# Kernel optimization log

Hardware: AMD Instinct MI355X
Metric: run time of the kernel (lower is better)

The kernel has to match this reference:

```python
import jax, jax.numpy as jnp
import numpy as np

B, T, D, H, L, F, V, BANDS = 16, 512, 1024, 8, 6, 4096, 30000, 16
RES = [1, 1, 2, 2, 4, 4, 8, 8]  # per-head K/V resolution schedule
HD = D // H


def setup_inputs() -> dict:
    key = jax.random.key(0)
    ks = iter(jax.random.split(key, 64))
    s = 0.02
    p = {
        "tokens": jax.random.randint(next(ks), (B, T), 0, V, dtype=jnp.int32),
        "embed": jax.random.normal(next(ks), (V, D), jnp.float32) * s,
        "pos_embed": jax.random.normal(next(ks), (T, D), jnp.float32) * s,
        "Wq": jax.random.normal(next(ks), (L, D, D), jnp.float32) * s,
        "bq": jnp.zeros((L, D), jnp.float32),
        "Wk": jax.random.normal(next(ks), (L, D, D), jnp.float32) * s,
        "bk": jnp.zeros((L, D), jnp.float32),
        "Wv": jax.random.normal(next(ks), (L, D, D), jnp.float32) * s,
        "bv": jnp.zeros((L, D), jnp.float32),
        "Wo": jax.random.normal(next(ks), (L, D, D), jnp.float32) * s,
        "bo": jnp.zeros((L, D), jnp.float32),
        "ln1_g": jnp.ones((L, D), jnp.float32),
        "ln1_b": jnp.zeros((L, D), jnp.float32),
        "ln2_g": jnp.ones((L, D), jnp.float32),
        "ln2_b": jnp.zeros((L, D), jnp.float32),
        "W1": jax.random.normal(next(ks), (L, D, F), jnp.float32) * s,
        "b1": jnp.zeros((L, F), jnp.float32),
        "W2": jax.random.normal(next(ks), (L, F, D), jnp.float32) * s,
        "b2": jnp.zeros((L, D), jnp.float32),
        "gates": jnp.ones((L, H, BANDS), jnp.float32),
        "lnf_g": jnp.ones((D,), jnp.float32),
        "lnf_b": jnp.zeros((D,), jnp.float32),
    }
    return p


def _ln(x, g, b, eps=1e-5):
    mu = jnp.mean(x, -1, keepdims=True)
    var = jnp.var(x, -1, keepdims=True)
    return (x - mu) * jax.lax.rsqrt(var + eps) * g + b


def _hfa_attention(x, Wq, bq, Wk, bk, Wv, bv, Wo, bo, gates_l):
    # x: [B,T,D]; per-head resolution schedule + spectral band gating.
    q = (x @ Wq + bq).reshape(B, T, H, HD).transpose(0, 2, 1, 3)  # [B,H,T,HD]
    k = (x @ Wk + bk).reshape(B, T, H, HD).transpose(0, 2, 1, 3)
    v = (x @ Wv + bv).reshape(B, T, H, HD).transpose(0, 2, 1, 3)
    nb = T // 2 + 1
    band_of_bin = (jnp.arange(nb) * BANDS) // nb  # map rfft bin -> spectral band
    scale = 1.0 / np.sqrt(HD)
    outs = []
    for h in range(H):
        r = RES[h]
        kh = k[:, h].reshape(B, T // r, r, HD).mean(2)  # pooled keys [B,T/r,HD]
        vh = v[:, h].reshape(B, T // r, r, HD).mean(2)
        scores = jnp.einsum("btd,bsd->bts", q[:, h], kh) * scale
        attn = jax.nn.softmax(scores, axis=-1)
        o = jnp.einsum("bts,bsd->btd", attn, vh)  # [B,T,HD]
        # spectral band gating along sequence axis
        g = gates_l[h][band_of_bin]  # [nb]
        f = jnp.fft.rfft(o, axis=1) * g[None, :, None]
        o = jnp.fft.irfft(f, n=T, axis=1)
        outs.append(o)
    out = jnp.concatenate(outs, axis=-1)  # [B,T,D]
    return out @ Wo + bo


def reference(tokens, embed, pos_embed, Wq, bq, Wk, bk, Wv, bv, Wo, bo,
              ln1_g, ln1_b, ln2_g, ln2_b, W1, b1, W2, b2, gates, lnf_g, lnf_b):
    x = embed[tokens] + pos_embed[jnp.arange(T)][None, :, :]  # [B,T,D]
    for l in range(L):
        h = _ln(x, ln1_g[l], ln1_b[l])
        x = x + _hfa_attention(h, Wq[l], bq[l], Wk[l], bk[l], Wv[l], bv[l],
                               Wo[l], bo[l], gates[l])
        h = _ln(x, ln2_g[l], ln2_b[l])
        ff = jax.nn.gelu(h @ W1[l] + b1[l], approximate=False) @ W2[l] + b2[l]
        x = x + ff
    return _ln(x, lnf_g, lnf_b)
```

## Files before the change

kernel.cpp:

```cpp
#include <hip/hip_runtime.h>
#include <hip/hip_bf16.h>
#include <math.h>

#define Bn 16
#define Tn 512
#define Dn 1024
#define Hn 8
#define Ln 6
#define Fn 4096
#define HDn 128

typedef __attribute__((ext_vector_type(8))) short short8;
typedef __attribute__((ext_vector_type(4))) float f32x4;

__device__ __forceinline__ float bf2f(unsigned short u){
  union{float f; unsigned int i;} c; c.i = ((unsigned int)u)<<16; return c.f;
}
__device__ __forceinline__ unsigned short f2bf(float f){
  union{float f; unsigned int i;} c; c.f=f;
  unsigned int r = c.i + 0x7fffu + ((c.i>>16)&1u);
  return (unsigned short)(r>>16);
}

#define GLOAD(gp, lp) __builtin_amdgcn_global_load_lds( \
    (const __attribute__((address_space(1))) void*)(const void*)(gp), \
    (__attribute__((address_space(3))) void*)(void*)(lp), 16, 0, 0)

__global__ __launch_bounds__(256) void embed_kernel(
    const int* __restrict__ tok, const float* __restrict__ emb,
    const float* __restrict__ pos, float* __restrict__ x){
  long row = blockIdx.x;
  int t = (int)(row & (Tn-1));
  int tk = tok[row];
  int d = threadIdx.x*4;
  float4 e = *(const float4*)(emb + (long)tk*Dn + d);
  float4 p = *(const float4*)(pos + (long)t*Dn + d);
  float4 r; r.x=e.x+p.x; r.y=e.y+p.y; r.z=e.z+p.z; r.w=e.w+p.w;
  *(float4*)(x + row*(long)Dn + d) = r;
}

template<int OUTBF>
__global__ __launch_bounds__(256) void ln_kernel(
    const float* __restrict__ x, const float* __restrict__ g,
    const float* __restrict__ b, void* __restrict__ outp){
  long row = blockIdx.x;
  const float* xr = x + row*(long)Dn;
  int tid = threadIdx.x;
  float4 v4 = *(const float4*)(xr + tid*4);
  float s  = v4.x+v4.y+v4.z+v4.w;
  float s2 = v4.x*v4.x + v4.y*v4.y + v4.z*v4.z + v4.w*v4.w;
  #pragma unroll
  for (int o=32;o;o>>=1){ s += __shfl_xor(s,o); s2 += __shfl_xor(s2,o); }
  __shared__ float rs[4], rs2[4];
  int w = tid>>6;
  if ((tid&63)==0){ rs[w]=s; rs2[w]=s2; }
  __syncthreads();
  s  = rs[0]+rs[1]+rs[2]+rs[3];
  s2 = rs2[0]+rs2[1]+rs2[2]+rs2[3];
  float mu  = s*(1.f/Dn);
  float var = s2*(1.f/Dn) - mu*mu;
  float rstd = rsqrtf(var + 1e-5f);
  float4 gg = *(const float4*)(g + tid*4);
  float4 bb = *(const float4*)(b + tid*4);
  float o0 = (v4.x-mu)*rstd*gg.x + bb.x;
  float o1 = (v4.y-mu)*rstd*gg.y + bb.y;
  float o2 = (v4.z-mu)*rstd*gg.z + bb.z;
  float o3 = (v4.w-mu)*rstd*gg.w + bb.w;
  if (OUTBF){
    unsigned short* o = (unsigned short*)outp + row*(long)Dn + tid*4;
    o[0]=f2bf(o0); o[1]=f2bf(o1); o[2]=f2bf(o2); o[3]=f2bf(o3);
  } else {
    float* o = (float*)outp + row*(long)Dn + tid*4;
    o[0]=o0; o[1]=o1; o[2]=o2; o[3]=o3;
  }
}

__global__ __launch_bounds__(256) void transpose_w(
    const float* __restrict__ W, unsigned short* __restrict__ WT, int Kd, int Nd){
  __shared__ float tile[32][33];
  long lofs = (long)blockIdx.z * Kd * Nd;
  int n0 = blockIdx.x*32, k0 = blockIdx.y*32;
  int tx = threadIdx.x & 31, ty = threadIdx.x >> 5;
  #pragma unroll
  for (int i=0;i<4;i++){
    int kk = k0 + ty + i*8;
    tile[ty+i*8][tx] = W[lofs + (long)kk*Nd + n0 + tx];
  }
  __syncthreads();
  #pragma unroll
  for (int i=0;i<4;i++){
    int nn = n0 + ty + i*8;
    WT[lofs + (long)nn*Kd + k0 + tx] = f2bf(tile[tx][ty+i*8]);
  }
}

__global__ __launch_bounds__(256) void pack_bias(
    const float* __restrict__ bq, const float* __restrict__ bk,
    const float* __restrict__ bv, float* __restrict__ bqkv){
  int i = blockIdx.x*256 + threadIdx.x;
  int l = i / (3*Dn); int r = i - l*3*Dn; int w = r / Dn; int d = r - w*Dn;
  const float* src = (w==0)? bq : ((w==1)? bk : bv);
  bqkv[i] = src[l*Dn + d];
}

__global__ __launch_bounds__(512) void ckern(
    const float* __restrict__ gates, float* __restrict__ cbuf){
  int lh = blockIdx.x;
  __shared__ float gb[16];
  if (threadIdx.x < 16) gb[threadIdx.x] = gates[lh*16 + threadIdx.x];
  __syncthreads();
  int m = threadIdx.x;
  float acc = gb[0];
  for (int j=1;j<256;j++){
    int band = (j*16)/257;
    int kmod = (j*m) & 511;
    acc += 2.f*gb[band]*cosf(1.2271846303085129e-2f * (float)kmod);
  }
  acc += gb[15] * ((m & 1) ? -1.f : 1.f);
  cbuf[lh*512 + m] = acc * (1.f/512.f);
}

__global__ __launch_bounds__(256) void gfill(
    const float* __restrict__ cbuf, unsigned short* __restrict__ G){
  long idx = (long)blockIdx.x*256 + threadIdx.x;
  int lh = (int)(idx >> 18);
  int rem = (int)(idx & 262143);
  int t = rem >> 9, s = rem & 511;
  G[idx] = f2bf(cbuf[lh*512 + ((t - s) & 511)]);
}

__global__ __launch_bounds__(256) void pool_kernel(
    const unsigned short* __restrict__ kin, const unsigned short* __restrict__ vin,
    unsigned short* __restrict__ kp, unsigned short* __restrict__ vTp){
  long idx = (long)blockIdx.x*256 + threadIdx.x;
  if (idx >= (long)Bn*1920*HDn) return;
  long rem = idx; int hh = 0; int S = 512;
  for (hh=0; hh<8; hh++){
    S = 512 >> (hh>>1);
    long seg = (long)Bn*S*HDn;
    if (rem < seg) break;
    rem -= seg;
  }
  int r = 512 / S;
  int d = (int)(rem % HDn);
  long t2 = rem / HDn;
  int s = (int)(t2 % S);
  int b = (int)(t2 / S);
  const unsigned short* kb = kin + ((long)(b*Tn + s*r))*Dn + hh*HDn + d;
  const unsigned short* vb = vin + ((long)(b*Tn + s*r))*Dn + hh*HDn + d;
  float ks=0.f, vs=0.f;
  for (int j=0;j<r;j++){ ks += bf2f(kb[(long)j*Dn]); vs += bf2f(vb[(long)j*Dn]); }
  float inv = 1.f/(float)r;
  int pref=0;
  for (int g2=0; g2<hh; g2++) pref += 512 >> (g2>>1);
  long segb = (long)Bn*HDn*pref;
  kp [segb + ((long)b*S + s)*HDn + d] = f2bf(ks*inv);
  vTp[segb + ((long)b*HDn + d)*S + s] = f2bf(vs*inv);
}

template<int S>
__global__ __launch_bounds__(64) void softmax_kernel(
    const float* __restrict__ sc, unsigned short* __restrict__ at){
  const int NV = S/64;
  long row = blockIdx.x;
  const float* r = sc + row*(long)S;
  int lane = threadIdx.x;
  float vals[NV];
  float mx = -1e30f;
  #pragma unroll
  for (int i=0;i<NV;i++){ vals[i] = r[lane + i*64] * 0.08838834764831845f; mx = fmaxf(mx, vals[i]); }
  #pragma unroll
  for (int o=32;o;o>>=1) mx = fmaxf(mx, __shfl_xor(mx, o));
  float sum = 0.f;
  #pragma unroll
  for (int i=0;i<NV;i++){ vals[i] = expf(vals[i]-mx); sum += vals[i]; }
  #pragma unroll
  for (int o=32;o;o>>=1) sum += __shfl_xor(sum, o);
  float inv = 1.f/sum;
  #pragma unroll
  for (int i=0;i<NV;i++) at[row*(long)S + lane + i*64] = f2bf(vals[i]*inv);
}

template<int MODE>
__global__ __launch_bounds__(256)
void gemm_kernel(const unsigned short* __restrict__ A, int lda, long sAb, long sAh,
                 const unsigned short* __restrict__ Bt, int ldb, long sBb, long sBh,
                 void* __restrict__ Cout, int ldc, long sCb, long sCh,
                 const float* __restrict__ bias, long sbias,
                 int zshift, int zmask,
                 int M, int N, int K)
{
  __shared__ unsigned short AB[2][2][128*64];
  int z = blockIdx.z;
  int zb = z & zmask, zh = z >> zshift;
  const unsigned short* Az = A + (long)zb*sAb + (long)zh*sAh;
  const unsigned short* Bz = Bt + (long)zb*sBb + (long)zh*sBh;
  const float* biasz = bias ? (bias + (long)zh*sbias) : nullptr;
  int m0 = blockIdx.y*128, n0 = blockIdx.x*128;
  int tid = threadIdx.x;
  int lane = tid & 63, wid = tid >> 6;
  int wm = wid >> 1, wn = wid & 1;
  f32x4 zero4 = {0.f,0.f,0.f,0.f};
  f32x4 acc[4][4];
  #pragma unroll
  for (int m=0;m<4;m++)
    #pragma unroll
    for (int n=0;n<4;n++)
      acc[m][n] = zero4;
  const int r16 = lane & 15, kq = lane >> 4;

  auto stage = [&](int buf, int k0){
    #pragma unroll
    for (int i=0;i<4;i++){
      int chunk = i*256 + tid;
      int row = chunk >> 3, c = chunk & 7;
      int cg = (c ^ (row & 7)) * 8;
      int gm = m0 + row; gm = gm < M ? gm : M-1;
      GLOAD(Az + (long)gm*lda + k0 + cg, AB[buf][0] + (i*256 + wid*64)*8);
    }
    #pragma unroll
    for (int i=0;i<4;i++){
      int chunk = i*256 + tid;
      int row = chunk >> 3, c = chunk & 7;
      int cg = (c ^ (row & 7)) * 8;
      int gn = n0 + row; gn = gn < N ? gn : N-1;
      GLOAD(Bz + (long)gn*ldb + k0 + cg, AB[buf][1] + (i*256 + wid*64)*8);
    }
  };

  int NT = K >> 6;
  stage(0, 0);
  for (int t = 0; t < NT; t++){
    if (t + 1 < NT){
      stage((t+1)&1, (t+1)*64);
      asm volatile("s_waitcnt vmcnt(8)" ::: "memory");
    } else {
      asm volatile("s_waitcnt vmcnt(0)" ::: "memory");
    }
    __builtin_amdgcn_s_barrier();
    const unsigned short* As = AB[t&1][0];
    const unsigned short* Bs = AB[t&1][1];
    #pragma unroll
    for (int kk=0; kk<64; kk+=32){
      short8 af[4], bfr[4];
      int kb = (kk + kq*8) * 2;
      #pragma unroll
      for (int m=0;m<4;m++){
        int row = wm*64 + m*16 + r16;
        af[m] = *(const short8*)((const char*)As + row*128 + (kb ^ ((row & 7) << 4)));
      }
      #pragma unroll
      for (int n=0;n<4;n++){
        int row = wn*64 + n*16 + r16;
        bfr[n] = *(const short8*)((const char*)Bs + row*128 + (kb ^ ((row & 7) << 4)));
      }
      #pragma unroll
      for (int m=0;m<4;m++)
        #pragma unroll
        for (int n=0;n<4;n++)
          acc[m][n] = __builtin_amdgcn_mfma_f32_16x16x32_bf16(af[m], bfr[n], acc[m][n], 0, 0, 0);
    }
    __builtin_amdgcn_s_barrier();
  }
  #pragma unroll
  for (int n=0;n<4;n++){
    int col = n0 + wn*64 + n*16 + r16;
    if (col >= N) continue;
    float bvv = 0.f;
    if (MODE != 0 && biasz != nullptr) bvv = biasz[col];
    #pragma unroll
    for (int m=0;m<4;m++){
      #pragma unroll
      for (int e=0;e<4;e++){
        int row = m0 + wm*64 + m*16 + kq*4 + e;
        if (row >= M) continue;
        float vv = acc[m][n][e] + bvv;
        long cidx = (long)zb*sCb + (long)zh*sCh + (long)row*ldc + col;
        if (MODE == 0)      ((float*)Cout)[cidx] = vv;
        else                ((unsigned short*)Cout)[cidx] = f2bf(vv);
      }
    }
  }
}

template<int MODE, int Mt, int Nt, int Kt, long SBH, long SCH, int BIASST>
__global__ __launch_bounds__(256)
void gemm_big(const unsigned short* __restrict__ A,
              const unsigned short* __restrict__ Bt,
              void* __restrict__ Cout,
              const float* __restrict__ bias)
{
  __shared__ char shraw[2][32768];
  int zh = blockIdx.z;
  const unsigned short* Bz = Bt + (long)zh*SBH;
  const float* biasz = bias + (long)zh*BIASST;
  constexpr int gx = Nt/128, gy = Mt/128, nwg = gx*gy;
  int lin  = blockIdx.y * gx + blockIdx.x;
  int nlin = (lin & 7) * (nwg >> 3) + (lin >> 3);
  int m0 = (nlin / gx) * 128, n0 = (nlin % gx) * 128;
  int tid = threadIdx.x;
  int lane = tid & 63, wid = tid >> 6;
  int wm = wid >> 1, wn = wid & 1;
  f32x4 zero4 = {0.f,0.f,0.f,0.f};
  f32x4 acc[4][4];
  #pragma unroll
  for (int m=0;m<4;m++)
    #pragma unroll
    for (int n=0;n<4;n++)
      acc[m][n] = zero4;
  const int r16 = lane & 15, kq = lane >> 4;

  const unsigned short* pA[4];
  const unsigned short* pB[4];
  #pragma unroll
  for (int i=0;i<4;i++){
    int chunk = i*256 + tid;
    int row = chunk >> 3, c = chunk & 7;
    int cg = (c ^ (row & 7)) * 8;
    pA[i] = A  + (long)(m0 + row)*Kt + cg;
    pB[i] = Bz + (long)(n0 + row)*Kt + cg;
  }
  auto stage = [&](int buf, int k0){
    unsigned short* As = (unsigned short*)shraw[buf];
    #pragma unroll
    for (int i=0;i<4;i++) GLOAD(pA[i] + k0, As + (i*256 + wid*64)*8);
    #pragma unroll
    for (int i=0;i<4;i++) GLOAD(pB[i] + k0, As + 8192 + (i*256 + wid*64)*8);
  };

  constexpr int NT = Kt/64;
  stage(0, 0);
  for (int t = 0; t < NT; t++){
    if (t + 1 < NT){
      stage((t+1)&1, (t+1)*64);
      asm volatile("s_waitcnt vmcnt(8)" ::: "memory");
    } else {
      asm volatile("s_waitcnt vmcnt(0)" ::: "memory");
    }
    __builtin_amdgcn_s_barrier();
    const unsigned short* As = (const unsigned short*)shraw[t&1];
    const unsigned short* Bs = As + 8192;
    #pragma unroll
    for (int kk=0; kk<64; kk+=32){
      short8 af[4], bfr[4];
      int kb = (kk + kq*8) * 2;
      #pragma unroll
      for (int m=0;m<4;m++){
        int row = wm*64 + m*16 + r16;
        af[m] = *(const short8*)((const char*)As + row*128 + (kb ^ ((row & 7) << 4)));
      }
      #pragma unroll
      for (int n=0;n<4;n++){
        int row = wn*64 + n*16 + r16;
        bfr[n] = *(const short8*)((const char*)Bs + row*128 + (kb ^ ((row & 7) << 4)));
      }
      #pragma unroll
      for (int m=0;m<4;m++)
        #pragma unroll
        for (int n=0;n<4;n++)
          acc[m][n] = __builtin_amdgcn_mfma_f32_16x16x32_bf16(af[m], bfr[n], acc[m][n], 0, 0, 0);
    }
    __builtin_amdgcn_s_barrier();
  }

  if (MODE == 1 || MODE == 2){
    unsigned short* shb = (unsigned short*)&shraw[0][0];
    #pragma unroll
    for (int n=0;n<4;n++){
      int col = wn*64 + n*16 + r16;
      float bvv = biasz[n0 + col];
      #pragma unroll
      for (int m=0;m<4;m++){
        #pragma unroll
        for (int e=0;e<4;e++){
          int row = wm*64 + m*16 + kq*4 + e;
          float vv = acc[m][n][e] + bvv;
          if (MODE == 2) vv = 0.5f*vv*(1.f + erff(vv*0.7071067811865475f));
          shb[row*136 + col] = f2bf(vv);
        }
      }
    }
    __syncthreads();
    #pragma unroll
    for (int i=0;i<8;i++){
      int chunk = i*256 + tid;
      int row = chunk >> 4, col = (chunk & 15)*8;
      short8 vv8 = *(const short8*)(shb + row*136 + col);
      *(short8*)((unsigned short*)Cout + (long)zh*SCH +
                 (long)(m0 + row)*Nt + n0 + col) = vv8;
    }
  } else {
    float* shf = (float*)&shraw[0][0];
    #pragma unroll
    for (int ph=0; ph<2; ph++){
      __syncthreads();
      if (wm == ph){
        #pragma unroll
        for (int n=0;n<4;n++){
          int col = wn*64 + n*16 + r16;
          float bvv = biasz[n0 + col];
          #pragma unroll
          for (int m=0;m<4;m++){
            #pragma unroll
            for (int e=0;e<4;e++){
              int rl = m*16 + kq*4 + e;
              shf[rl*136 + col] = acc[m][n][e] + bvv;
            }
          }
        }
      }
      __syncthreads();
      #pragma unroll
      for (int i=0;i<8;i++){
        int chunk = i*256 + tid;
        int row = chunk >> 5, col = (chunk & 31)*4;
        float4 vv = *(const float4*)(shf + row*136 + col);
        float* cp = (float*)Cout + (long)(m0 + ph*64 + row)*Nt + n0 + col;
        float4 o = *(const float4*)cp;
        o.x += vv.x; o.y += vv.y; o.z += vv.z; o.w += vv.w;
        *(float4*)cp = o;
      }
    }
  }
}

extern "C" void kernel_launch(void* const* d_in, const int* in_sizes, int n_in,
                              void* d_out, int out_size, void* d_ws, size_t ws_size,
                              hipStream_t stream){
  const int*   tokens = (const int*)  d_in[0];
  const float* embedp = (const float*)d_in[1];
  const float* pos    = (const float*)d_in[2];
  const float* Wq  = (const float*)d_in[3];
  const float* bq  = (const float*)d_in[4];
  const float* Wk  = (const float*)d_in[5];
  const float* bk  = (const float*)d_in[6];
  const float* Wv  = (const float*)d_in[7];
  const float* bv  = (const float*)d_in[8];
  const float* Wo  = (const float*)d_in[9];
  const float* bo  = (const float*)d_in[10];
  const float* ln1g= (const float*)d_in[11];
  const float* ln1b= (const float*)d_in[12];
  const float* ln2g= (const float*)d_in[13];
  const float* ln2b= (const float*)d_in[14];
  const float* W1  = (const float*)d_in[15];
  const float* b1  = (const float*)d_in[16];
  const float* W2  = (const float*)d_in[17];
  const float* b2  = (const float*)d_in[18];
  const float* gates=(const float*)d_in[19];
  const float* lnfg= (const float*)d_in[20];
  const float* lnfb= (const float*)d_in[21];
  float* out = (float*)d_out;

  char* base = (char*)d_ws;
  size_t off = 0;
  auto take = [&](size_t bytes)->char*{
    char* p = base + off;
    off = (off + bytes + 255) & ~(size_t)255;
    return p;
  };
  unsigned short* WqT = (unsigned short*)take((size_t)Ln*Dn*Dn*2);
  unsigned short* WkT = (unsigned short*)take((size_t)Ln*Dn*Dn*2);
  unsigned short* WvT = (unsigned short*)take((size_t)Ln*Dn*Dn*2);
  unsigned short* WoT = (unsigned short*)take((size_t)Ln*Dn*Dn*2);
  unsigned short* W1T = (unsigned short*)take((size_t)Ln*Dn*Fn*2);
  unsigned short* W2T = (unsigned short*)take((size_t)Ln*Dn*Fn*2);
  unsigned short* G   = (unsigned short*)take((size_t)Ln*Hn*Tn*Tn*2);
  float*          cbuf= (float*)take((size_t)Ln*Hn*Tn*4);
  float*          bqkv= (float*)take((size_t)Ln*3*Dn*4);
  float*          x   = (float*)take((size_t)Bn*Tn*Dn*4);
  unsigned short* hbuf= (unsigned short*)take((size_t)Bn*Tn*Dn*2);
  unsigned short* q   = (unsigned short*)take((size_t)Bn*Tn*Dn*2);
  unsigned short* k   = (unsigned short*)take((size_t)Bn*Tn*Dn*2);
  unsigned short* v   = (unsigned short*)take((size_t)Bn*Tn*Dn*2);
  unsigned short* kp  = (unsigned short*)take((size_t)Bn*1920*HDn*2);
  unsigned short* vTp = (unsigned short*)take((size_t)Bn*1920*HDn*2);
  unsigned short* oT  = (unsigned short*)take((size_t)2*Bn*HDn*Tn*2);
  unsigned short* ao  = (unsigned short*)take((size_t)Bn*Tn*Dn*2);
  unsigned short* ff1 = (unsigned short*)take((size_t)Bn*Tn*Fn*2);
  if (off > ws_size) return;
  float*          scoresA = (float*)ff1;
  unsigned short* attnA   = (unsigned short*)(scoresA + (size_t)2*Bn*Tn*512);

  transpose_w<<<dim3(Dn/32, Dn/32, Ln), 256, 0, stream>>>(Wq, WqT, Dn, Dn);
  transpose_w<<<dim3(Dn/32, Dn/32, Ln), 256, 0, stream>>>(Wk, WkT, Dn, Dn);
  transpose_w<<<dim3(Dn/32, Dn/32, Ln), 256, 0, stream>>>(Wv, WvT, Dn, Dn);
  transpose_w<<<dim3(Dn/32, Dn/32, Ln), 256, 0, stream>>>(Wo, WoT, Dn, Dn);
  transpose_w<<<dim3(Fn/32, Dn/32, Ln), 256, 0, stream>>>(W1, W1T, Dn, Fn);
  transpose_w<<<dim3(Dn/32, Fn/32, Ln), 256, 0, stream>>>(W2, W2T, Fn, Dn);
  pack_bias<<<(Ln*3*Dn)/256, 256, 0, stream>>>(bq, bk, bv, bqkv);
  ckern<<<Ln*Hn, 512, 0, stream>>>(gates, cbuf);
  gfill<<<(Ln*Hn*Tn*Tn)/256, 256, 0, stream>>>(cbuf, G);
  embed_kernel<<<Bn*Tn, 256, 0, stream>>>(tokens, embedp, pos, x);

  const int pref[8] = {0,512,1024,1280,1536,1664,1792,1856};
  const int MT = Bn*Tn;

  for (int l=0; l<Ln; l++){
    ln_kernel<1><<<MT, 256, 0, stream>>>(x, ln1g + l*Dn, ln1b + l*Dn, hbuf);
    gemm_big<1, 8192, Dn, Dn, (long)Ln*Dn*Dn, (long)Bn*Tn*Dn, Dn>
        <<<dim3(Dn/128, MT/128, 3), 256, 0, stream>>>(
        hbuf, WqT + (size_t)l*Dn*Dn, q, bqkv + (size_t)l*3*Dn);
    pool_kernel<<<((long)Bn*1920*HDn + 255)/256, 256, 0, stream>>>(k, v, kp, vTp);

    for (int g=0; g<4; g++){
      int h0 = 2*g;
      int S  = Tn >> g;
      long koff = (long)Bn*HDn*pref[h0];
      gemm_kernel<0><<<dim3((S+127)/128, Tn/128, 32), 256, 0, stream>>>(
          q + h0*HDn, Dn, (long)Tn*Dn, (long)HDn,
          kp + koff, HDn, (long)S*HDn, (long)Bn*HDn*S,
          scoresA, S, (long)Tn*S, (long)Bn*Tn*S,
          nullptr, 0L, 4, 15,
          Tn, S, HDn);
      switch (S){
        case 512: softmax_kernel<512><<<2*MT, 64, 0, stream>>>(scoresA, attnA); break;
        case 256: softmax_kernel<256><<<2*MT, 64, 0, stream>>>(scoresA, attnA); break;
        case 128: softmax_kernel<128><<<2*MT, 64, 0, stream>>>(scoresA, attnA); break;
        default:  softmax_kernel< 64><<<2*MT, 64, 0, stream>>>(scoresA, attnA); break;
      }
      gemm_kernel<1><<<dim3(Tn/128, HDn/128, 32), 256, 0, stream>>>(
          vTp + koff, S, (long)HDn*S, (long)Bn*HDn*S,
          attnA, S, (long)Tn*S, (long)Bn*Tn*S,
          oT, Tn, (long)HDn*Tn, (long)Bn*HDn*Tn,
          nullptr, 0L, 4, 15,
          HDn, Tn, S);
      gemm_kernel<1><<<dim3(HDn/128, Tn/128, 32), 256, 0, stream>>>(
          G + (size_t)(l*Hn + h0)*Tn*Tn, Tn, 0L, (long)Tn*Tn,
          oT, Tn, (long)HDn*Tn, (long)Bn*HDn*Tn,
          ao + h0*HDn, Dn, (long)Tn*Dn, (long)HDn,
          nullptr, 0L, 4, 15,
          Tn, HDn, Tn);
    }
    gemm_big<3, 8192, Dn, Dn, 0L, 0L, 0>
        <<<dim3(Dn/128, MT/128, 1), 256, 0, stream>>>(
        ao, WoT + (size_t)l*Dn*Dn, x, bo + l*Dn);
    ln_kernel<1><<<MT, 256, 0, stream>>>(x, ln2g + l*Dn, ln2b + l*Dn, hbuf);
    gemm_big<2, 8192, Fn, Dn, 0L, 0L, 0>
        <<<dim3(Fn/128, MT/128, 1), 256, 0, stream>>>(
        hbuf, W1T + (size_t)l*Dn*Fn, ff1, b1 + l*Fn);
    gemm_big<3, 8192, Dn, Fn, 0L, 0L, 0>
        <<<dim3(Dn/128, MT/128, 1), 256, 0, stream>>>(
        ff1, W2T + (size_t)l*Dn*Fn, x, b2 + l*Dn);
  }
  ln_kernel<0><<<MT, 256, 0, stream>>>(x, lnfg, lnfb, out);
}
```

Baseline: 3.279 ms.

## Add 256x256-tile pipelined GEMM kernel for QKV and FFN1 projections

Adds a new 512-thread GEMM kernel with 256x256 output tiles, triple-buffered A and double-buffered B staging through LDS via global_load_lds, explicit vmcnt waits and s_setprio around the MFMA blocks. It replaces the 128x128 gemm_big for the fused QKV projection (which now writes Q/K/V as a split across z from one 3072-wide launch) and for the FFN1 GELU GEMM. gemm_big is trimmed to the accumulate-only mode and loses its grouped block-index swizzle. The larger tiles raise data reuse per loaded byte but use 160KB LDS and many accumulator registers per block, which limits occupancy and can leave CUs idle at the tail (384 and 512 blocks).

After: 3.465 ms. +5.7%, slower.

```diff
diff --git a/kernel.cpp b/kernel.cpp
--- a/kernel.cpp
+++ b/kernel.cpp
@@ -294,10 +294,7 @@
   int zh = blockIdx.z;
   const unsigned short* Bz = Bt + (long)zh*SBH;
   const float* biasz = bias + (long)zh*BIASST;
-  constexpr int gx = Nt/128, gy = Mt/128, nwg = gx*gy;
-  int lin  = blockIdx.y * gx + blockIdx.x;
-  int nlin = (lin & 7) * (nwg >> 3) + (lin >> 3);
-  int m0 = (nlin / gx) * 128, n0 = (nlin % gx) * 128;
+  int m0 = blockIdx.y*128, n0 = blockIdx.x*128;
   int tid = threadIdx.x;
   int lane = tid & 63, wid = tid >> 6;
   int wm = wid >> 1, wn = wid & 1;
@@ -363,20 +360,22 @@
     __builtin_amdgcn_s_barrier();
   }
 
-  if (MODE == 1 || MODE == 2){
-    unsigned short* shb = (unsigned short*)&shraw[0][0];
-    #pragma unroll
-    for (int n=0;n<4;n++){
-      int col = wn*64 + n*16 + r16;
-      float bvv = biasz[n0 + col];
-      #pragma unroll
-      for (int m=0;m<4;m++){
+  float* shf = (float*)&shraw[0][0];
+  #pragma unroll
+  for (int ph=0; ph<2; ph++){
+    __syncthreads();
+    if (wm == ph){
+      #pragma unroll
+      for (int n=0;n<4;n++){
+        int col = wn*64 + n*16 + r16;
+        float bvv = biasz[n0 + col];
         #pragma unroll
-        for (int e=0;e<4;e++){
-          int row = wm*64 + m*16 + kq*4 + e;
-          float vv = acc[m][n][e] + bvv;
-          if (MODE == 2) vv = 0.5f*vv*(1.f + erff(vv*0.7071067811865475f));
-          shb[row*136 + col] = f2bf(vv);
+        for (int m=0;m<4;m++){
+          #pragma unroll
+          for (int e=0;e<4;e++){
+            int rl = m*16 + kq*4 + e;
+            shf[rl*136 + col] = acc[m][n][e] + bvv;
+          }
         }
       }
     }
@@ -384,43 +383,143 @@
     #pragma unroll
     for (int i=0;i<8;i++){
       int chunk = i*256 + tid;
-      int row = chunk >> 4, col = (chunk & 15)*8;
-      short8 vv8 = *(const short8*)(shb + row*136 + col);
-      *(short8*)((unsigned short*)Cout + (long)zh*SCH +
-                 (long)(m0 + row)*Nt + n0 + col) = vv8;
-    }
+      int row = chunk >> 5, col = (chunk & 31)*4;
+      float4 vv = *(const float4*)(shf + row*136 + col);
+      float* cp = (float*)Cout + (long)(m0 + ph*64 + row)*Nt + n0 + col;
+      float4 o = *(const float4*)cp;
+      o.x += vv.x; o.y += vv.y; o.z += vv.z; o.w += vv.w;
+      *(float4*)cp = o;
+    }
+  }
+}
+
+template<int MODE, int Mt, int Nt, int Kt, int SPLITZ, long SBH, long SCH>
+__global__ __launch_bounds__(512, 2)
+void gemm256(const unsigned short* __restrict__ A,
+             const unsigned short* __restrict__ Bt,
+             void* __restrict__ Cout,
+             const float* __restrict__ bias)
+{
+  __shared__ char lds[163840];
+  int tid = threadIdx.x;
+  int lane = tid & 63, w = tid >> 6;
+  int wm = w >> 2, wn = w & 3;
+  int r16 = lane & 15, kq = lane >> 4;
+  int m0 = blockIdx.y * 256, n0 = blockIdx.x * 256;
+
+  const unsigned short* Bz = SPLITZ ? (Bt + (long)(n0 >> 10) * SBH) : Bt;
+  int nloc = SPLITZ ? (n0 & 1023) : n0;
+
+  const unsigned short* pA[4];
+  const unsigned short* pB[4];
+  #pragma unroll
+  for (int j=0;j<4;j++){
+    int chunk = j*512 + tid;
+    int row = chunk >> 3, c = chunk & 7;
+    int cg = (c ^ (row & 7)) * 8;
+    pA[j] = A  + (long)(m0 + row)*Kt + cg;
+    pB[j] = Bz + (long)(nloc + row)*Kt + cg;
+  }
+  auto stageA = [&](int buf, int k0){
+    char* dst = lds + buf*32768;
+    #pragma unroll
+    for (int j=0;j<4;j++) GLOAD(pA[j] + k0, dst + (j*512 + w*64)*16);
+  };
+  auto stageB = [&](int buf, int k0){
+    char* dst = lds + 98304 + buf*32768;
+    #pragma unroll
+    for (int j=0;j<4;j++) GLOAD(pB[j] + k0, dst + (j*512 + w*64)*16);
+  };
+
+  f32x4 acc[8][4];
+  f32x4 z4 = {0.f,0.f,0.f,0.f};
+  #pragma unroll
+  for (int m=0;m<8;m++)
+    #pragma unroll
+    for (int n=0;n<4;n++)
+      acc[m][n] = z4;
+
+  constexpr int nt = Kt/64;
+  stageB(0, 0);
+  stageA(0, 0);
+  if (nt > 1){
+    stageA(1, 64);
+    asm volatile("s_waitcnt vmcnt(4)" ::: "memory");
   } else {
-    float* shf = (float*)&shraw[0][0];
-    #pragma unroll
-    for (int ph=0; ph<2; ph++){
-      __syncthreads();
-      if (wm == ph){
+    asm volatile("s_waitcnt vmcnt(0)" ::: "memory");
+  }
+  asm volatile("s_barrier" ::: "memory");
+
+  for (int T = 0; T < nt; T++){
+    const char* Ac = lds + (T%3)*32768;
+    const char* Bc = lds + 98304 + (T&1)*32768;
+    #pragma unroll
+    for (int ks=0; ks<2; ks++){
+      short8 af[8], bfv[4];
+      int kb = (ks*32 + kq*8)*2;
+      #pragma unroll
+      for (int m=0;m<8;m++){
+        int row = wm*128 + m*16 + r16;
+        af[m] = *(const short8*)(Ac + row*128 + (kb ^ ((row&7)<<4)));
+      }
+      #pragma unroll
+      for (int n=0;n<4;n++){
+        int row = wn*64 + n*16 + r16;
+        bfv[n] = *(const short8*)(Bc + row*128 + (kb ^ ((row&7)<<4)));
+      }
+      if (ks == 0){ if (T+1 < nt) stageB((T+1)&1, (T+1)*64); }
+      else        { if (T+2 < nt) stageA((T+2)%3, (T+2)*64); }
+      asm volatile("s_barrier" ::: "memory");
+      __builtin_amdgcn_s_setprio(1);
+      #pragma unroll
+      for (int m=0;m<8;m++)
         #pragma unroll
-        for (int n=0;n<4;n++){
-          int col = wn*64 + n*16 + r16;
-          float bvv = biasz[n0 + col];
+        for (int n=0;n<4;n++)
+          acc[m][n] = __builtin_amdgcn_mfma_f32_16x16x32_bf16(af[m], bfv[n], acc[m][n], 0, 0, 0);
+      __builtin_amdgcn_s_setprio(0);
+      if (ks == 1){
+        if (T+2 < nt)      asm volatile("s_waitcnt vmcnt(4)" ::: "memory");
+        else if (T+1 < nt) asm volatile("s_waitcnt vmcnt(0)" ::: "memory");
+      }
+      asm volatile("s_barrier" ::: "memory");
+    }
+  }
+
+  unsigned short* ep = (unsigned short*)lds;
+  #pragma unroll
+  for (int ph=0; ph<2; ph++){
+    if (wm == ph){
+      #pragma unroll
+      for (int n=0;n<4;n++){
+        int col = wn*64 + n*16 + r16;
+        float bvv = bias[n0 + col];
+        #pragma unroll
+        for (int m=0;m<8;m++){
           #pragma unroll
-          for (int m=0;m<4;m++){
-            #pragma unroll
-            for (int e=0;e<4;e++){
-              int rl = m*16 + kq*4 + e;
-              shf[rl*136 + col] = acc[m][n][e] + bvv;
-            }
+          for (int e=0;e<4;e++){
+            int rl = m*16 + kq*4 + e;
+            float vv = acc[m][n][e] + bvv;
+            if (MODE == 2) vv = 0.5f*vv*(1.f + erff(vv*0.7071067811865475f));
+            ep[rl*264 + col] = f2bf(vv);
           }
         }
       }
-      __syncthreads();
-      #pragma unroll
-      for (int i=0;i<8;i++){
-        int chunk = i*256 + tid;
-        int row = chunk >> 5, col = (chunk & 31)*4;
-        float4 vv = *(const float4*)(shf + row*136 + col);
-        float* cp = (float*)Cout + (long)(m0 + ph*64 + row)*Nt + n0 + col;
-        float4 o = *(const float4*)cp;
-        o.x += vv.x; o.y += vv.y; o.z += vv.z; o.w += vv.w;
-        *(float4*)cp = o;
-      }
-    }
+    }
+    asm volatile("s_barrier" ::: "memory");
+    #pragma unroll
+    for (int i=0;i<8;i++){
+      int chunk = i*512 + tid;
+      int row = chunk >> 5, col = (chunk & 31)*8;
+      short8 v8 = *(const short8*)(ep + row*264 + col);
+      int grow = m0 + ph*128 + row;
+      if (SPLITZ){
+        int cg = n0 + col; int zz = cg >> 10; int cl = cg & 1023;
+        *(short8*)((unsigned short*)Cout + (long)zz*SCH + (long)grow*1024 + cl) = v8;
+      } else {
+        *(short8*)((unsigned short*)Cout + (long)grow*Nt + n0 + col) = v8;
+      }
+    }
+    asm volatile("s_barrier" ::: "memory");
   }
 }
 
@@ -497,8 +596,8 @@
 
   for (int l=0; l<Ln; l++){
     ln_kernel<1><<<MT, 256, 0, stream>>>(x, ln1g + l*Dn, ln1b + l*Dn, hbuf);
-    gemm_big<1, 8192, Dn, Dn, (long)Ln*Dn*Dn, (long)Bn*Tn*Dn, Dn>
-        <<<dim3(Dn/128, MT/128, 3), 256, 0, stream>>>(
+    gemm256<1, 8192, 3072, 1024, 1, (long)Ln*Dn*Dn, (long)Bn*Tn*Dn>
+        <<<dim3(12, 32), 512, 0, stream>>>(
         hbuf, WqT + (size_t)l*Dn*Dn, q, bqkv + (size_t)l*3*Dn);
     pool_kernel<<<((long)Bn*1920*HDn + 255)/256, 256, 0, stream>>>(k, v, kp, vTp);
 
@@ -535,8 +634,8 @@
         <<<dim3(Dn/128, MT/128, 1), 256, 0, stream>>>(
         ao, WoT + (size_t)l*Dn*Dn, x, bo + l*Dn);
     ln_kernel<1><<<MT, 256, 0, stream>>>(x, ln2g + l*Dn, ln2b + l*Dn, hbuf);
-    gemm_big<2, 8192, Fn, Dn, 0L, 0L, 0>
-        <<<dim3(Fn/128, MT/128, 1), 256, 0, stream>>>(
+    gemm256<2, 8192, Fn, 1024, 0, 0L, 0L>
+        <<<dim3(16, 32), 512, 0, stream>>>(
         hbuf, W1T + (size_t)l*Dn*Fn, ff1, b1 + l*Fn);
     gemm_big<3, 8192, Dn, Fn, 0L, 0L, 0>
         <<<dim3(Dn/128, MT/128, 1), 256, 0, stream>>>(
```
